# Performance work log

Hardware: AMD Instinct MI355X
Metric: run time of the kernel (lower is better)

Reference implementation:

```python
import jax, jax.numpy as jnp
import numpy as np

B, N, M = 2, 2048, 2048
Q_DIM = 1024
HEADS = 8
DIM_HEAD = 64
INNER = HEADS * DIM_HEAD  # 512


def setup_inputs() -> dict:
    key = jax.random.key(0)
    ks = jax.random.split(key, 7)
    s_in = 1.0 / np.sqrt(Q_DIM)
    s_out = 1.0 / np.sqrt(INNER)
    return {
        "x": jax.random.normal(ks[0], (B, N, Q_DIM), dtype=jnp.float32),
        "context": jax.random.normal(ks[1], (B, M, Q_DIM), dtype=jnp.float32),
        "Wq": jax.random.normal(ks[2], (Q_DIM, INNER), dtype=jnp.float32) * s_in,
        "Wk": jax.random.normal(ks[3], (Q_DIM, INNER), dtype=jnp.float32) * s_in,
        "Wv": jax.random.normal(ks[4], (Q_DIM, INNER), dtype=jnp.float32) * s_in,
        "Wo": jax.random.normal(ks[5], (INNER, Q_DIM), dtype=jnp.float32) * s_out,
        "bo": jax.random.normal(ks[6], (Q_DIM,), dtype=jnp.float32) * 0.01,
    }


def reference(x, context, Wq, Wk, Wv, Wo, bo):
    scale = DIM_HEAD ** (-0.5)
    # projections, split heads: [b, n, inner] -> [b, h, n, d]
    def split_heads(t):
        b, n, _ = t.shape
        return t.reshape(b, n, HEADS, DIM_HEAD).transpose(0, 2, 1, 3)
    q = split_heads(x @ Wq)
    k = split_heads(context @ Wk)
    v = split_heads(context @ Wv)
    sim = jnp.einsum('bhid,bhjd->bhij', q, k) * scale  # [b,h,n,m] full score matrix
    attn = jax.nn.softmax(sim, axis=-1)
    out = jnp.einsum('bhij,bhjd->bhid', attn, v)       # [b,h,n,d]
    out = out.transpose(0, 2, 1, 3).reshape(x.shape[0], x.shape[1], INNER)
    return out @ Wo + bo
```

## Files before the change

kernel.cpp:

```cpp
#include <hip/hip_runtime.h>

typedef __attribute__((ext_vector_type(8))) short short8;
typedef __attribute__((ext_vector_type(4))) short bf16x4;
typedef __attribute__((ext_vector_type(4))) float floatx4;
typedef __attribute__((ext_vector_type(4))) float f32x4;

__device__ __forceinline__ short f2bf(float f) {
    union { float f; unsigned u; } v;
    v.f = f;
    unsigned r = v.u + 0x7fffu + ((v.u >> 16) & 1u);
    return (short)(r >> 16);
}
__device__ __forceinline__ short8 cvt8(f32x4 a, f32x4 b) {
    short8 r;
    r[0] = f2bf(a[0]); r[1] = f2bf(a[1]); r[2] = f2bf(a[2]); r[3] = f2bf(a[3]);
    r[4] = f2bf(b[0]); r[5] = f2bf(b[1]); r[6] = f2bf(b[2]); r[7] = f2bf(b[3]);
    return r;
}
__device__ __forceinline__ bf16x4 pack4(float a, float b, float c, float d) {
    union { float f; unsigned u; } x;
    unsigned ua, ub, uc, ud;
    x.f = a; ua = (x.u + 0x8000u) >> 16;
    x.f = b; ub = (x.u + 0x8000u) >> 16;
    x.f = c; uc = (x.u + 0x8000u) >> 16;
    x.f = d; ud = (x.u + 0x8000u) >> 16;
    union { bf16x4 s; unsigned u2[2]; } r;
    r.u2[0] = ua | (ub << 16);
    r.u2[1] = uc | (ud << 16);
    return r.s;
}

#define MFMA_BF16(a, b, c) __builtin_amdgcn_mfma_f32_16x16x32_bf16((a), (b), (c), 0, 0, 0)

__device__ __forceinline__ floatx4 mfma16(bf16x4 a, bf16x4 b, floatx4 c) {
#if __has_builtin(__builtin_amdgcn_mfma_f32_16x16x16bf16_1k)
    return __builtin_amdgcn_mfma_f32_16x16x16bf16_1k(a, b, c, 0, 0, 0);
#else
    floatx4 d;
    asm volatile("v_mfma_f32_16x16x16_bf16 %0, %1, %2, %3"
                 : "=&v"(d) : "v"(a), "v"(b), "v"(c));
    return d;
#endif
}

__device__ __forceinline__ float fast_exp2(float x) {
#if __has_builtin(__builtin_amdgcn_exp2f)
    return __builtin_amdgcn_exp2f(x);
#else
    return exp2f(x);
#endif
}

#define QSCALE_LOG2E 0.18033688011112042f

__global__ __launch_bounds__(256) void transpose_all(const float* __restrict__ Wq,
                                                     const float* __restrict__ Wk,
                                                     const float* __restrict__ Wv,
                                                     const float* __restrict__ Wo,
                                                     short* __restrict__ WqT,
                                                     short* __restrict__ WkT,
                                                     short* __restrict__ WvT,
                                                     short* __restrict__ WoT) {
    const int z = blockIdx.z;
    const float* src = (z == 0) ? Wq : (z == 1) ? Wk : (z == 2) ? Wv : Wo;
    short* dst = (z == 0) ? WqT : (z == 1) ? WkT : (z == 2) ? WvT : WoT;
    const int R = (z < 3) ? 1024 : 512;
    const int C = (z < 3) ? 512 : 1024;
    const int c0 = blockIdx.x * 32;
    const int r0 = blockIdx.y * 32;
    if (c0 >= C || r0 >= R) return;
    __shared__ float tile[32][33];
    const int tx = threadIdx.x;
    const int ty = threadIdx.y;
#pragma unroll
    for (int i = 0; i < 32; i += 8)
        tile[ty + i][tx] = src[(r0 + ty + i) * C + c0 + tx];
    __syncthreads();
#pragma unroll
    for (int i = 0; i < 32; i += 8)
        dst[(c0 + ty + i) * R + r0 + tx] = f2bf(tile[tx][ty + i]);
}

__global__ __launch_bounds__(256, 4) void gemm_qkv(const float* __restrict__ x,
                                                   const float* __restrict__ ctx,
                                                   const short* __restrict__ WqT,
                                                   const short* __restrict__ WkT,
                                                   const short* __restrict__ WvT,
                                                   short* __restrict__ Qw,
                                                   short* __restrict__ Kw,
                                                   short* __restrict__ Vtw) {
    const int z = blockIdx.z;
    const float* A  = (z == 0) ? x : ctx;
    const short* WT = (z == 0) ? WqT : (z == 1) ? WkT : WvT;
    const int tid = threadIdx.x;
    const int w = tid >> 6;
    const int lane = tid & 63;
    const int quad = lane >> 4, ln = lane & 15;
    const int wr = w >> 1, wc = w & 1;
    const int row0 = blockIdx.x * 64;
    const int col0 = blockIdx.y * 128;

    __shared__ __align__(16) short Alds[2][64][32];
    __shared__ __align__(16) short Blds[2][128][32];

    const int srow = tid >> 2;
    const int scol = (tid & 3) * 8;
    const float* aG = A + (size_t)(row0 + srow) * 1024 + scol;
    const short* bG0 = WT + (size_t)(col0 + srow) * 1024 + scol;
    const short* bG1 = WT + (size_t)(col0 + srow + 64) * 1024 + scol;

    floatx4 acc[2][4] = {};

    {
        f32x4 a0 = *(const f32x4*)(aG);
        f32x4 a1 = *(const f32x4*)(aG + 4);
        *(short8*)(&Alds[0][srow][scol]) = cvt8(a0, a1);
        *(short8*)(&Blds[0][srow][scol]) = *(const short8*)(bG0);
        *(short8*)(&Blds[0][srow + 64][scol]) = *(const short8*)(bG1);
    }
    __syncthreads();

    const int nsteps = 1024 / 32;
    for (int it = 0; it < nsteps; ++it) {
        f32x4 a0, a1;
        short8 br0, br1;
        const bool more = (it + 1 < nsteps);
        if (more) {
            const int kk = (it + 1) * 32;
            a0  = *(const f32x4*)(aG + kk);
            a1  = *(const f32x4*)(aG + kk + 4);
            br0 = *(const short8*)(bG0 + kk);
            br1 = *(const short8*)(bG1 + kk);
        }
        const int b = it & 1;
        short8 af[2], bf4[4];
#pragma unroll
        for (int i = 0; i < 2; ++i)
            af[i] = *(const short8*)(&Alds[b][wr * 32 + i * 16 + ln][quad * 8]);
#pragma unroll
        for (int t = 0; t < 4; ++t)
            bf4[t] = *(const short8*)(&Blds[b][wc * 64 + t * 16 + ln][quad * 8]);
#pragma unroll
        for (int i = 0; i < 2; ++i)
#pragma unroll
            for (int t = 0; t < 4; ++t)
                acc[i][t] = MFMA_BF16(af[i], bf4[t], acc[i][t]);
        if (more) {
            const int nb = (it + 1) & 1;
            *(short8*)(&Alds[nb][srow][scol]) = cvt8(a0, a1);
            *(short8*)(&Blds[nb][srow][scol]) = br0;
            *(short8*)(&Blds[nb][srow + 64][scol]) = br1;
        }
        __syncthreads();
    }

    const float oscale = (z == 0) ? QSCALE_LOG2E : 1.0f;
    short* dst = (z == 0) ? Qw : (z == 1) ? Kw : Vtw;
#pragma unroll
    for (int i = 0; i < 2; ++i)
#pragma unroll
        for (int t = 0; t < 4; ++t)
#pragma unroll
            for (int r = 0; r < 4; ++r) {
                const int R = row0 + wr * 32 + i * 16 + quad * 4 + r;
                const int C = col0 + wc * 64 + t * 16 + ln;
                const int b = R >> 11, n = R & 2047;
                const int h = C >> 6, d = C & 63;
                const short val = f2bf(acc[i][t][r] * oscale);
                if (z < 2)
                    dst[((b * 8 + h) * 2048 + n) * 64 + d] = val;
                else
                    dst[((b * 8 + h) * 64 + d) * 2048 + n] = val;
            }
}

__global__ __launch_bounds__(256, 2) void attn_kernel(const short* __restrict__ Q,
                                                      const short* __restrict__ K,
                                                      const short* __restrict__ Vt,
                                                      short* __restrict__ Aw) {
    const int tid = threadIdx.x;
    const int w = tid >> 6;
    const int lane = tid & 63;
    const int quad = lane >> 4;
    const int ln = lane & 15;
    const int q0 = blockIdx.x * 64;
    const int bh = blockIdx.y;

    __shared__ __align__(16) short klds[2][64][72];
    __shared__ __align__(16) short vlds[2][64][72];

    const short* Qbh = Q + bh * 2048 * 64;
    const short* Kbh = K + bh * 2048 * 64;
    const short* Vbh = Vt + bh * 64 * 2048;

    short8 qf[2];
    {
        const int qrow = q0 + w * 16 + ln;
        qf[0] = *(const short8*)(Qbh + qrow * 64 + quad * 8);
        qf[1] = *(const short8*)(Qbh + qrow * 64 + 32 + quad * 8);
    }

    floatx4 ot[4] = {};
    float lp = 0.f;

    const int sr = tid >> 3;
    const int sc = (tid & 7) * 8;

    auto computeTile = [&](int b) {
        short8 kf[8];
#pragma unroll
        for (int t = 0; t < 4; ++t)
#pragma unroll
            for (int ks = 0; ks < 2; ++ks)
                kf[t * 2 + ks] = *(const short8*)(&klds[b][t * 16 + ln][ks * 32 + quad * 8]);
        bf16x4 vf[16];
#pragma unroll
        for (int dt = 0; dt < 4; ++dt)
#pragma unroll
            for (int t = 0; t < 4; ++t)
                vf[dt * 4 + t] = *(const bf16x4*)(&vlds[b][dt * 16 + ln][t * 16 + quad * 4]);

        floatx4 s[4] = {};
#pragma unroll
        for (int ks = 0; ks < 2; ++ks)
#pragma unroll
            for (int t = 0; t < 4; ++t)
                s[t] = MFMA_BF16(kf[t * 2 + ks], qf[ks], s[t]);

        bf16x4 pf[4];
#pragma unroll
        for (int t = 0; t < 4; ++t) {
            float p0 = fast_exp2(s[t][0]);
            float p1 = fast_exp2(s[t][1]);
            float p2 = fast_exp2(s[t][2]);
            float p3 = fast_exp2(s[t][3]);
            lp += (p0 + p1) + (p2 + p3);
            pf[t] = pack4(p0, p1, p2, p3);
        }
#pragma unroll
        for (int t = 0; t < 4; ++t)
#pragma unroll
            for (int dt = 0; dt < 4; ++dt)
                ot[dt] = mfma16(vf[dt * 4 + t], pf[t], ot[dt]);
    };

    const int nt = 2048 / 64;

    {
        short8 k0 = *(const short8*)(Kbh + tid * 8);
        short8 k1 = *(const short8*)(Kbh + (tid + 256) * 8);
        short8 v0 = *(const short8*)(Vbh + sr * 2048 + sc);
        short8 v1 = *(const short8*)(Vbh + (sr + 32) * 2048 + sc);
        *(short8*)(&klds[0][sr][sc]) = k0;
        *(short8*)(&klds[0][sr + 32][sc]) = k1;
        *(short8*)(&vlds[0][sr][sc]) = v0;
        *(short8*)(&vlds[0][sr + 32][sc]) = v1;
    }
    __syncthreads();

    for (int it = 0; it < nt; ++it) {
        short8 k0, k1, v0, v1;
        const bool more = (it + 1 < nt);
        if (more) {
            const int jn = (it + 1) * 64;
            k0 = *(const short8*)(Kbh + jn * 64 + tid * 8);
            k1 = *(const short8*)(Kbh + jn * 64 + (tid + 256) * 8);
            v0 = *(const short8*)(Vbh + sr * 2048 + jn + sc);
            v1 = *(const short8*)(Vbh + (sr + 32) * 2048 + jn + sc);
        }
        computeTile(it & 1);
        if (more) {
            const int nb = (it + 1) & 1;
            *(short8*)(&klds[nb][sr][sc]) = k0;
            *(short8*)(&klds[nb][sr + 32][sc]) = k1;
            *(short8*)(&vlds[nb][sr][sc]) = v0;
            *(short8*)(&vlds[nb][sr + 32][sc]) = v1;
        }
        __syncthreads();
    }

    lp += __shfl_xor(lp, 16);
    lp += __shfl_xor(lp, 32);
    const float invL = 1.0f / lp;

    const int n = q0 + w * 16 + ln;
    const int b = bh >> 3, h = bh & 7;
    short* abase = Aw + ((size_t)(b * 2048 + n) * 512) + h * 64 + quad * 4;
#pragma unroll
    for (int dt = 0; dt < 4; ++dt)
        *(bf16x4*)(abase + dt * 16) =
            pack4(ot[dt][0] * invL, ot[dt][1] * invL, ot[dt][2] * invL, ot[dt][3] * invL);
}

__global__ __launch_bounds__(256, 4) void gemm_final(const short* __restrict__ A,
                                                     const short* __restrict__ WoT,
                                                     const float* __restrict__ bias,
                                                     float* __restrict__ out) {
    const int tid = threadIdx.x;
    const int w = tid >> 6;
    const int lane = tid & 63;
    const int quad = lane >> 4, ln = lane & 15;
    const int wr = w >> 1, wc = w & 1;
    const int row0 = blockIdx.x * 64;
    const int col0 = blockIdx.y * 128;

    __shared__ __align__(16) short Alds[2][64][32];
    __shared__ __align__(16) short Blds[2][128][32];

    const int srow = tid >> 2;
    const int scol = (tid & 3) * 8;
    const short* aG = A + (size_t)(row0 + srow) * 512 + scol;
    const short* bG0 = WoT + (size_t)(col0 + srow) * 512 + scol;
    const short* bG1 = WoT + (size_t)(col0 + srow + 64) * 512 + scol;

    floatx4 acc[2][4] = {};

    {
        *(short8*)(&Alds[0][srow][scol]) = *(const short8*)(aG);
        *(short8*)(&Blds[0][srow][scol]) = *(const short8*)(bG0);
        *(short8*)(&Blds[0][srow + 64][scol]) = *(const short8*)(bG1);
    }
    __syncthreads();

    const int nsteps = 512 / 32;
    for (int it = 0; it < nsteps; ++it) {
        short8 ar, br0, br1;
        const bool more = (it + 1 < nsteps);
        if (more) {
            const int kk = (it + 1) * 32;
            ar  = *(const short8*)(aG + kk);
            br0 = *(const short8*)(bG0 + kk);
            br1 = *(const short8*)(bG1 + kk);
        }
        const int b = it & 1;
        short8 af[2], bf4[4];
#pragma unroll
        for (int i = 0; i < 2; ++i)
            af[i] = *(const short8*)(&Alds[b][wr * 32 + i * 16 + ln][quad * 8]);
#pragma unroll
        for (int t = 0; t < 4; ++t)
            bf4[t] = *(const short8*)(&Blds[b][wc * 64 + t * 16 + ln][quad * 8]);
#pragma unroll
        for (int i = 0; i < 2; ++i)
#pragma unroll
            for (int t = 0; t < 4; ++t)
                acc[i][t] = MFMA_BF16(af[i], bf4[t], acc[i][t]);
        if (more) {
            const int nb = (it + 1) & 1;
            *(short8*)(&Alds[nb][srow][scol]) = ar;
            *(short8*)(&Blds[nb][srow][scol]) = br0;
            *(short8*)(&Blds[nb][srow + 64][scol]) = br1;
        }
        __syncthreads();
    }

#pragma unroll
    for (int i = 0; i < 2; ++i)
#pragma unroll
        for (int t = 0; t < 4; ++t)
#pragma unroll
            for (int r = 0; r < 4; ++r) {
                const int R = row0 + wr * 32 + i * 16 + quad * 4 + r;
                const int C = col0 + wc * 64 + t * 16 + ln;
                out[(size_t)R * 1024 + C] = acc[i][t][r] + bias[C];
            }
}

extern "C" void kernel_launch(void* const* d_in, const int* in_sizes, int n_in,
                              void* d_out, int out_size, void* d_ws, size_t ws_size,
                              hipStream_t stream) {
    const float* x   = (const float*)d_in[0];
    const float* ctx = (const float*)d_in[1];
    const float* Wq  = (const float*)d_in[2];
    const float* Wk  = (const float*)d_in[3];
    const float* Wv  = (const float*)d_in[4];
    const float* Wo  = (const float*)d_in[5];
    const float* bo  = (const float*)d_in[6];
    float* out = (float*)d_out;

    char* ws = (char*)d_ws;
    size_t off = 0;
    auto alloc = [&](size_t bytes) { char* p = ws + off; off += (bytes + 255) & ~(size_t)255; return p; };

    short* WqT  = (short*)alloc(512 * 1024 * 2);
    short* WkT  = (short*)alloc(512 * 1024 * 2);
    short* WvT  = (short*)alloc(512 * 1024 * 2);
    short* WoT  = (short*)alloc(1024 * 512 * 2);
    short* Qw   = (short*)alloc((size_t)16 * 2048 * 64 * 2);
    short* Kw   = (short*)alloc((size_t)16 * 2048 * 64 * 2);
    short* Vtw  = (short*)alloc((size_t)16 * 2048 * 64 * 2);
    short* Aw   = (short*)alloc((size_t)4096 * 512 * 2);

    transpose_all<<<dim3(32, 32, 4), dim3(32, 8), 0, stream>>>(Wq, Wk, Wv, Wo, WqT, WkT, WvT, WoT);

    gemm_qkv<<<dim3(64, 4, 3), 256, 0, stream>>>(x, ctx, WqT, WkT, WvT, Qw, Kw, Vtw);

    attn_kernel<<<dim3(32, 16), 256, 0, stream>>>(Qw, Kw, Vtw, Aw);

    gemm_final<<<dim3(64, 8), 256, 0, stream>>>(Aw, WoT, bo, out);
}
```

Baseline: 171.8 us.

## Load GEMM weight fragments directly from global and stage A in larger LDS chunks

```diff
diff --git a/kernel.cpp b/kernel.cpp
--- a/kernel.cpp
+++ b/kernel.cpp
@@ -52,6 +52,8 @@
 }
 
 #define QSCALE_LOG2E 0.18033688011112042f
+
+#define APAD 136
 
 __global__ __launch_bounds__(256) void transpose_all(const float* __restrict__ Wq,
                                                      const float* __restrict__ Wk,
@@ -81,7 +83,7 @@
         dst[(c0 + ty + i) * R + r0 + tx] = f2bf(tile[tx][ty + i]);
 }
 
-__global__ __launch_bounds__(256, 4) void gemm_qkv(const float* __restrict__ x,
+__global__ __launch_bounds__(256, 3) void gemm_qkv(const float* __restrict__ x,
                                                    const float* __restrict__ ctx,
                                                    const short* __restrict__ WqT,
                                                    const short* __restrict__ WkT,
@@ -100,58 +102,59 @@
     const int row0 = blockIdx.x * 64;
     const int col0 = blockIdx.y * 128;
 
-    __shared__ __align__(16) short Alds[2][64][32];
-    __shared__ __align__(16) short Blds[2][128][32];
-
-    const int srow = tid >> 2;
-    const int scol = (tid & 3) * 8;
-    const float* aG = A + (size_t)(row0 + srow) * 1024 + scol;
-    const short* bG0 = WT + (size_t)(col0 + srow) * 1024 + scol;
-    const short* bG1 = WT + (size_t)(col0 + srow + 64) * 1024 + scol;
+    __shared__ __align__(16) short Alds[2][64][APAD];
+
+    const int arow = tid >> 2;
+    const int aseg = tid & 3;
+    const float* aG = A + (size_t)(row0 + arow) * 1024 + aseg * 32;
+    const short* bG[4];
+#pragma unroll
+    for (int t = 0; t < 4; ++t)
+        bG[t] = WT + (size_t)(col0 + wc * 64 + t * 16 + ln) * 1024 + quad * 8;
 
     floatx4 acc[2][4] = {};
-
-    {
-        f32x4 a0 = *(const f32x4*)(aG);
-        f32x4 a1 = *(const f32x4*)(aG + 4);
-        *(short8*)(&Alds[0][srow][scol]) = cvt8(a0, a1);
-        *(short8*)(&Blds[0][srow][scol]) = *(const short8*)(bG0);
-        *(short8*)(&Blds[0][srow + 64][scol]) = *(const short8*)(bG1);
-    }
+    f32x4 areg[8];
+
+    auto loadA = [&](int c) {
+#pragma unroll
+        for (int i = 0; i < 8; ++i)
+            areg[i] = *(const f32x4*)(aG + c * 128 + i * 4);
+    };
+    auto writeA = [&](int buf) {
+#pragma unroll
+        for (int i = 0; i < 4; ++i)
+            *(short8*)(&Alds[buf][arow][aseg * 32 + i * 8]) = cvt8(areg[2 * i], areg[2 * i + 1]);
+    };
+
+    loadA(0);
+    writeA(0);
     __syncthreads();
 
-    const int nsteps = 1024 / 32;
-    for (int it = 0; it < nsteps; ++it) {
-        f32x4 a0, a1;
-        short8 br0, br1;
-        const bool more = (it + 1 < nsteps);
+    const int nch = 1024 / 128;
+    for (int c = 0; c < nch; ++c) {
+        const int buf = c & 1;
+        const bool more = (c + 1 < nch);
+        if (more) loadA(c + 1);
+#pragma unroll
+        for (int s = 0; s < 4; ++s) {
+            const int k = c * 128 + s * 32;
+            short8 bf4[4];
+#pragma unroll
+            for (int t = 0; t < 4; ++t) bf4[t] = *(const short8*)(bG[t] + k);
+            short8 af[2];
+#pragma unroll
+            for (int i = 0; i < 2; ++i)
+                af[i] = *(const short8*)(&Alds[buf][wr * 32 + i * 16 + ln][s * 32 + quad * 8]);
+#pragma unroll
+            for (int i = 0; i < 2; ++i)
+#pragma unroll
+                for (int t = 0; t < 4; ++t)
+                    acc[i][t] = MFMA_BF16(af[i], bf4[t], acc[i][t]);
+        }
         if (more) {
-            const int kk = (it + 1) * 32;
-            a0  = *(const f32x4*)(aG + kk);
-            a1  = *(const f32x4*)(aG + kk + 4);
-            br0 = *(const short8*)(bG0 + kk);
-            br1 = *(const short8*)(bG1 + kk);
-        }
-        const int b = it & 1;
-        short8 af[2], bf4[4];
-#pragma unroll
-        for (int i = 0; i < 2; ++i)
-            af[i] = *(const short8*)(&Alds[b][wr * 32 + i * 16 + ln][quad * 8]);
-#pragma unroll
-        for (int t = 0; t < 4; ++t)
-            bf4[t] = *(const short8*)(&Blds[b][wc * 64 + t * 16 + ln][quad * 8]);
-#pragma unroll
-        for (int i = 0; i < 2; ++i)
-#pragma unroll
-            for (int t = 0; t < 4; ++t)
-                acc[i][t] = MFMA_BF16(af[i], bf4[t], acc[i][t]);
-        if (more) {
-            const int nb = (it + 1) & 1;
-            *(short8*)(&Alds[nb][srow][scol]) = cvt8(a0, a1);
-            *(short8*)(&Blds[nb][srow][scol]) = br0;
-            *(short8*)(&Blds[nb][srow + 64][scol]) = br1;
-        }
-        __syncthreads();
+            writeA(buf ^ 1);
+            __syncthreads();
+        }
     }
 
     const float oscale = (z == 0) ? QSCALE_LOG2E : 1.0f;
@@ -292,7 +295,7 @@
             pack4(ot[dt][0] * invL, ot[dt][1] * invL, ot[dt][2] * invL, ot[dt][3] * invL);
 }
 
-__global__ __launch_bounds__(256, 4) void gemm_final(const short* __restrict__ A,
+__global__ __launch_bounds__(256, 2) void gemm_final(const short* __restrict__ A,
                                                      const short* __restrict__ WoT,
                                                      const float* __restrict__ bias,
                                                      float* __restrict__ out) {
@@ -304,54 +307,59 @@
     const int row0 = blockIdx.x * 64;
     const int col0 = blockIdx.y * 128;
 
-    __shared__ __align__(16) short Alds[2][64][32];
-    __shared__ __align__(16) short Blds[2][128][32];
-
-    const int srow = tid >> 2;
-    const int scol = (tid & 3) * 8;
-    const short* aG = A + (size_t)(row0 + srow) * 512 + scol;
-    const short* bG0 = WoT + (size_t)(col0 + srow) * 512 + scol;
-    const short* bG1 = WoT + (size_t)(col0 + srow + 64) * 512 + scol;
+    __shared__ __align__(16) short Alds[2][64][APAD];
+
+    const int arow = tid >> 2;
+    const int aseg = tid & 3;
+    const short* aG = A + (size_t)(row0 + arow) * 512 + aseg * 32;
+    const short* bG[4];
+#pragma unroll
+    for (int t = 0; t < 4; ++t)
+        bG[t] = WoT + (size_t)(col0 + wc * 64 + t * 16 + ln) * 512 + quad * 8;
 
     floatx4 acc[2][4] = {};
-
-    {
-        *(short8*)(&Alds[0][srow][scol]) = *(const short8*)(aG);
-        *(short8*)(&Blds[0][srow][scol]) = *(const short8*)(bG0);
-        *(short8*)(&Blds[0][srow + 64][scol]) = *(const short8*)(bG1);
-    }
+    short8 areg[4];
+
+    auto loadA = [&](int c) {
+#pragma unroll
+        for (int i = 0; i < 4; ++i)
+            areg[i] = *(const short8*)(aG + c * 128 + i * 8);
+    };
+    auto writeA = [&](int buf) {
+#pragma unroll
+        for (int i = 0; i < 4; ++i)
+            *(short8*)(&Alds[buf][arow][aseg * 32 + i * 8]) = areg[i];
+    };
+
+    loadA(0);
+    writeA(0);
     __syncthreads();
 
-    const int nsteps = 512 / 32;
-    for (int it = 0; it < nsteps; ++it) {
-        short8 ar, br0, br1;
-        const bool more = (it + 1 < nsteps);
+    const int nch = 512 / 128;
+    for (int c = 0; c < nch; ++c) {
+        const int buf = c & 1;
+        const bool more = (c + 1 < nch);
+        if (more) loadA(c + 1);
+#pragma unroll
+        for (int s = 0; s < 4; ++s) {
+            const int k = c * 128 + s * 32;
+            short8 bf4[4];
+#pragma unroll
+            for (int t = 0; t < 4; ++t) bf4[t] = *(const short8*)(bG[t] + k);
+            short8 af[2];
+#pragma unroll
+            for (int i = 0; i < 2; ++i)
+                af[i] = *(const short8*)(&Alds[buf][wr * 32 + i * 16 + ln][s * 32 + quad * 8]);
+#pragma unroll
+            for (int i = 0; i < 2; ++i)
+#pragma unroll
+                for (int t = 0; t < 4; ++t)
+                    acc[i][t] = MFMA_BF16(af[i], bf4[t], acc[i][t]);
+        }
         if (more) {
-            const int kk = (it + 1) * 32;
-            ar  = *(const short8*)(aG + kk);
-            br0 = *(const short8*)(bG0 + kk);
-            br1 = *(const short8*)(bG1 + kk);
-        }
-        const int b = it & 1;
-        short8 af[2], bf4[4];
-#pragma unroll
-        for (int i = 0; i < 2; ++i)
-            af[i] = *(const short8*)(&Alds[b][wr * 32 + i * 16 + ln][quad * 8]);
-#pragma unroll
-        for (int t = 0; t < 4; ++t)
-            bf4[t] = *(const short8*)(&Blds[b][wc * 64 + t * 16 + ln][quad * 8]);
-#pragma unroll
-        for (int i = 0; i < 2; ++i)
-#pragma unroll
-            for (int t = 0; t < 4; ++t)
-                acc[i][t] = MFMA_BF16(af[i], bf4[t], acc[i][t]);
-        if (more) {
-            const int nb = (it + 1) & 1;
-            *(short8*)(&Alds[nb][srow][scol]) = ar;
-            *(short8*)(&Blds[nb][srow][scol]) = br0;
-            *(short8*)(&Blds[nb][srow + 64][scol]) = br1;
-        }
-        __syncthreads();
+            writeA(buf ^ 1);
+            __syncthreads();
+        }
     }
 
 #pragma unroll
```

Measured after the change: 214.4 us. 24.8% more time.

## Deepen GEMM prefetch to two stages and pad LDS tiles against bank conflicts

Applied to the files above, without the earlier changes.

```diff
diff --git a/kernel.cpp b/kernel.cpp
--- a/kernel.cpp
+++ b/kernel.cpp
@@ -52,6 +52,8 @@
 }
 
 #define QSCALE_LOG2E 0.18033688011112042f
+
+#define TPAD 40
 
 __global__ __launch_bounds__(256) void transpose_all(const float* __restrict__ Wq,
                                                      const float* __restrict__ Wk,
@@ -81,7 +83,7 @@
         dst[(c0 + ty + i) * R + r0 + tx] = f2bf(tile[tx][ty + i]);
 }
 
-__global__ __launch_bounds__(256, 4) void gemm_qkv(const float* __restrict__ x,
+__global__ __launch_bounds__(256, 3) void gemm_qkv(const float* __restrict__ x,
                                                    const float* __restrict__ ctx,
                                                    const short* __restrict__ WqT,
                                                    const short* __restrict__ WkT,
@@ -100,8 +102,8 @@
     const int row0 = blockIdx.x * 64;
     const int col0 = blockIdx.y * 128;
 
-    __shared__ __align__(16) short Alds[2][64][32];
-    __shared__ __align__(16) short Blds[2][128][32];
+    __shared__ __align__(16) short Alds[2][64][TPAD];
+    __shared__ __align__(16) short Blds[2][128][TPAD];
 
     const int srow = tid >> 2;
     const int scol = (tid & 3) * 8;
@@ -110,47 +112,44 @@
     const short* bG1 = WT + (size_t)(col0 + srow + 64) * 1024 + scol;
 
     floatx4 acc[2][4] = {};
-
-    {
-        f32x4 a0 = *(const f32x4*)(aG);
-        f32x4 a1 = *(const f32x4*)(aG + 4);
-        *(short8*)(&Alds[0][srow][scol]) = cvt8(a0, a1);
-        *(short8*)(&Blds[0][srow][scol]) = *(const short8*)(bG0);
-        *(short8*)(&Blds[0][srow + 64][scol]) = *(const short8*)(bG1);
-    }
+    f32x4 aR[2][2];
+    short8 bR[2][2];
+
+    auto loadStep = [&](int it, int set) {
+        const int kk = it * 32;
+        aR[set][0] = *(const f32x4*)(aG + kk);
+        aR[set][1] = *(const f32x4*)(aG + kk + 4);
+        bR[set][0] = *(const short8*)(bG0 + kk);
+        bR[set][1] = *(const short8*)(bG1 + kk);
+    };
+    auto writeStep = [&](int buf, int set) {
+        *(short8*)(&Alds[buf][srow][scol]) = cvt8(aR[set][0], aR[set][1]);
+        *(short8*)(&Blds[buf][srow][scol]) = bR[set][0];
+        *(short8*)(&Blds[buf][srow + 64][scol]) = bR[set][1];
+    };
+
+    loadStep(0, 0);
+    writeStep(0, 0);
+    loadStep(1, 1);
     __syncthreads();
 
     const int nsteps = 1024 / 32;
     for (int it = 0; it < nsteps; ++it) {
-        f32x4 a0, a1;
-        short8 br0, br1;
-        const bool more = (it + 1 < nsteps);
-        if (more) {
-            const int kk = (it + 1) * 32;
-            a0  = *(const f32x4*)(aG + kk);
-            a1  = *(const f32x4*)(aG + kk + 4);
-            br0 = *(const short8*)(bG0 + kk);
-            br1 = *(const short8*)(bG1 + kk);
-        }
-        const int b = it & 1;
+        const int buf = it & 1;
+        if (it + 2 < nsteps) loadStep(it + 2, it & 1);
+        if (it + 1 < nsteps) writeStep(buf ^ 1, (it + 1) & 1);
         short8 af[2], bf4[4];
 #pragma unroll
         for (int i = 0; i < 2; ++i)
-            af[i] = *(const short8*)(&Alds[b][wr * 32 + i * 16 + ln][quad * 8]);
-#pragma unroll
-        for (int t = 0; t < 4; ++t)
-            bf4[t] = *(const short8*)(&Blds[b][wc * 64 + t * 16 + ln][quad * 8]);
+            af[i] = *(const short8*)(&Alds[buf][wr * 32 + i * 16 + ln][quad * 8]);
+#pragma unroll
+        for (int t = 0; t < 4; ++t)
+            bf4[t] = *(const short8*)(&Blds[buf][wc * 64 + t * 16 + ln][quad * 8]);
 #pragma unroll
         for (int i = 0; i < 2; ++i)
 #pragma unroll
             for (int t = 0; t < 4; ++t)
                 acc[i][t] = MFMA_BF16(af[i], bf4[t], acc[i][t]);
-        if (more) {
-            const int nb = (it + 1) & 1;
-            *(short8*)(&Alds[nb][srow][scol]) = cvt8(a0, a1);
-            *(short8*)(&Blds[nb][srow][scol]) = br0;
-            *(short8*)(&Blds[nb][srow + 64][scol]) = br1;
-        }
         __syncthreads();
     }
 
@@ -292,7 +291,7 @@
             pack4(ot[dt][0] * invL, ot[dt][1] * invL, ot[dt][2] * invL, ot[dt][3] * invL);
 }
 
-__global__ __launch_bounds__(256, 4) void gemm_final(const short* __restrict__ A,
+__global__ __launch_bounds__(256, 3) void gemm_final(const short* __restrict__ A,
                                                      const short* __restrict__ WoT,
                                                      const float* __restrict__ bias,
                                                      float* __restrict__ out) {
@@ -304,8 +303,8 @@
     const int row0 = blockIdx.x * 64;
     const int col0 = blockIdx.y * 128;
 
-    __shared__ __align__(16) short Alds[2][64][32];
-    __shared__ __align__(16) short Blds[2][128][32];
+    __shared__ __align__(16) short Alds[2][64][TPAD];
+    __shared__ __align__(16) short Blds[2][128][TPAD];
 
     const int srow = tid >> 2;
     const int scol = (tid & 3) * 8;
@@ -314,43 +313,43 @@
     const short* bG1 = WoT + (size_t)(col0 + srow + 64) * 512 + scol;
 
     floatx4 acc[2][4] = {};
-
-    {
-        *(short8*)(&Alds[0][srow][scol]) = *(const short8*)(aG);
-        *(short8*)(&Blds[0][srow][scol]) = *(const short8*)(bG0);
-        *(short8*)(&Blds[0][srow + 64][scol]) = *(const short8*)(bG1);
-    }
+    short8 aR[2];
+    short8 bR[2][2];
+
+    auto loadStep = [&](int it, int set) {
+        const int kk = it * 32;
+        aR[set]    = *(const short8*)(aG + kk);
+        bR[set][0] = *(const short8*)(bG0 + kk);
+        bR[set][1] = *(const short8*)(bG1 + kk);
+    };
+    auto writeStep = [&](int buf, int set) {
+        *(short8*)(&Alds[buf][srow][scol]) = aR[set];
+        *(short8*)(&Blds[buf][srow][scol]) = bR[set][0];
+        *(short8*)(&Blds[buf][srow + 64][scol]) = bR[set][1];
+    };
+
+    loadStep(0, 0);
+    writeStep(0, 0);
+    loadStep(1, 1);
     __syncthreads();
 
     const int nsteps = 512 / 32;
     for (int it = 0; it < nsteps; ++it) {
-        short8 ar, br0, br1;
-        const bool more = (it + 1 < nsteps);
-        if (more) {
-            const int kk = (it + 1) * 32;
-            ar  = *(const short8*)(aG + kk);
-            br0 = *(const short8*)(bG0 + kk);
-            br1 = *(const short8*)(bG1 + kk);
-        }
-        const int b = it & 1;
+        const int buf = it & 1;
+        if (it + 2 < nsteps) loadStep(it + 2, it & 1);
+        if (it + 1 < nsteps) writeStep(buf ^ 1, (it + 1) & 1);
         short8 af[2], bf4[4];
 #pragma unroll
         for (int i = 0; i < 2; ++i)
-            af[i] = *(const short8*)(&Alds[b][wr * 32 + i * 16 + ln][quad * 8]);
-#pragma unroll
-        for (int t = 0; t < 4; ++t)
-            bf4[t] = *(const short8*)(&Blds[b][wc * 64 + t * 16 + ln][quad * 8]);
+            af[i] = *(const short8*)(&Alds[buf][wr * 32 + i * 16 + ln][quad * 8]);
+#pragma unroll
+        for (int t = 0; t < 4; ++t)
+            bf4[t] = *(const short8*)(&Blds[buf][wc * 64 + t * 16 + ln][quad * 8]);
 #pragma unroll
         for (int i = 0; i < 2; ++i)
 #pragma unroll
             for (int t = 0; t < 4; ++t)
                 acc[i][t] = MFMA_BF16(af[i], bf4[t], acc[i][t]);
-        if (more) {
-            const int nb = (it + 1) & 1;
-            *(short8*)(&Alds[nb][srow][scol]) = ar;
-            *(short8*)(&Blds[nb][srow][scol]) = br0;
-            *(short8*)(&Blds[nb][srow + 64][scol]) = br1;
-        }
         __syncthreads();
     }
 
```

Result: no change. 168.9 us (-1.7%).
